# Kernel optimization log

Hardware: AMD Instinct MI355X
Metric: run time of the kernel (lower is better)

Reference implementation:

```python
import jax, jax.numpy as jnp
import numpy as np

LIDAR_MAX_X = 32.0
LIDAR_MAX_Y = 32.0


def bilinear_grid_sample(value, grid):
    """torch.nn.functional.grid_sample, mode='bilinear', padding_mode='zeros',
    align_corners=False.
    value: (B, C, H, W); grid: (B, Q, P, 2) in [-1, 1] (x=width, y=height).
    Returns (B, C, Q, P)."""
    B, C, H, W = value.shape
    x = (grid[..., 0] + 1.0) * (W / 2) - 0.5  # (B,Q,P) unnormalized col
    y = (grid[..., 1] + 1.0) * (H / 2) - 0.5  # (B,Q,P) unnormalized row
    x0 = jnp.floor(x)
    y0 = jnp.floor(y)
    x1 = x0 + 1.0
    y1 = y0 + 1.0
    wx1 = x - x0
    wx0 = 1.0 - wx1
    wy1 = y - y0
    wy0 = 1.0 - wy1
    vflat = value.reshape(B, C, H * W)

    def gather(ix, iy):
        valid = (ix >= 0) & (ix <= W - 1) & (iy >= 0) & (iy <= H - 1)
        ixc = jnp.clip(ix, 0, W - 1).astype(jnp.int32)
        iyc = jnp.clip(iy, 0, H - 1).astype(jnp.int32)
        idx = iyc * W + ixc  # (B,Q,P)
        g = jax.vmap(lambda v, i: v[:, i])(vflat, idx)  # (B,C,Q,P)
        return g * valid[:, None, :, :].astype(value.dtype)

    out = (gather(x0, y0) * (wx0 * wy0)[:, None]
           + gather(x1, y0) * (wx1 * wy0)[:, None]
           + gather(x0, y1) * (wx0 * wy1)[:, None]
           + gather(x1, y1) * (wx1 * wy1)[:, None])
    return out


def setup_inputs() -> dict:
    key = jax.random.key(0)
    ks = jax.random.split(key, 10)
    bs, Q, P, D = 16, 1024, 8, 256
    Cin, H, W = 64, 128, 128
    queries = jax.random.normal(ks[0], (bs, Q, D), dtype=jnp.float32)
    # scale so trajectory points span the +/-32m BEV extent
    traj_points = jax.random.normal(ks[1], (bs, Q, P, 2), dtype=jnp.float32) * 20.0
    bev_feature = jax.random.normal(ks[2], (bs, Cin, H, W), dtype=jnp.float32)
    spatial_shape = jnp.array([H, W], dtype=jnp.int64)
    attn_w = jax.random.normal(ks[3], (P, D), dtype=jnp.float32) * 0.02
    attn_b = jnp.zeros((P,), dtype=jnp.float32)
    conv_w = jax.random.normal(ks[4], (256, Cin, 3, 3), dtype=jnp.float32) * 0.05
    conv_b = jnp.zeros((256,), dtype=jnp.float32)
    out_w = jax.random.normal(ks[5], (D, D), dtype=jnp.float32) * (1.0 / np.sqrt(D))
    out_b = jnp.zeros((D,), dtype=jnp.float32)
    return {"queries": queries, "traj_points": traj_points,
            "bev_feature": bev_feature, "spatial_shape": spatial_shape,
            "attn_w": attn_w, "attn_b": attn_b,
            "conv_w": conv_w, "conv_b": conv_b,
            "out_w": out_w, "out_b": out_b}


def reference(queries, traj_points, bev_feature, spatial_shape,
              attn_w, attn_b, conv_w, conv_b, out_w, out_b):
    # normalize trajectory to [-1,1] and swap (y,x) -> (x,y) grid order
    grid = jnp.stack([traj_points[..., 1] / LIDAR_MAX_X,
                      traj_points[..., 0] / LIDAR_MAX_Y], axis=-1)  # (bs,Q,P,2)
    # per-query attention over the P sampled points
    attn = jax.nn.softmax(
        jnp.einsum('bqd,pd->bqp', queries, attn_w) + attn_b, axis=-1)  # (bs,Q,P)
    # value projection: 3x3 conv + ReLU
    value = jax.lax.conv_general_dilated(
        bev_feature, conv_w, window_strides=(1, 1),
        padding=((1, 1), (1, 1)),
        dimension_numbers=('NCHW', 'OIHW', 'NCHW'))
    value = jax.nn.relu(value + conv_b[None, :, None, None])  # (bs,256,H,W)
    sampled = bilinear_grid_sample(value, grid)  # (bs,256,Q,P)
    out = jnp.einsum('bcqp,bqp->bqc', sampled, attn)  # weighted sum + permute
    out = jnp.einsum('bqc,dc->bqd', out, out_w) + out_b
    # dropout is identity in eval mode
    return out + queries
```

## Files before the change

### kernel.cpp

```cpp
#include <hip/hip_runtime.h>
#include <stdint.h>


typedef __attribute__((ext_vector_type(8))) short short8;
typedef __attribute__((ext_vector_type(4))) float f32x4;

__device__ __forceinline__ unsigned short f2bf(float f) {
  union { float f; unsigned int u; } v; v.f = f;
  unsigned int r = (v.u + 0x7FFFu + ((v.u >> 16) & 1u)) >> 16;
  return (unsigned short)r;
}
__device__ __forceinline__ float bf2f(unsigned short h) {
  union { unsigned int u; float f; } v; v.u = ((unsigned int)h) << 16;
  return v.f;
}

__device__ __forceinline__ void gload_lds16(const void* g, void* l) {
  __builtin_amdgcn_global_load_lds(
      (const __attribute__((address_space(1))) unsigned int*)g,
      (__attribute__((address_space(3))) unsigned int*)l, 16, 0, 0);
}

__global__ __launch_bounds__(256) void k1_transpose(const float* __restrict__ bev,
                                                    unsigned short* __restrict__ nhwc) {
  __shared__ __align__(16) float lds[64 * 32 * 4];
  const int b = blockIdx.x >> 7, y = blockIdx.x & 127;
  const int t = threadIdx.x;
  const float* src = bev + (size_t)(b * 64) * 16384 + y * 128;
#pragma unroll
  for (int k = 0; k < 8; ++k) {
    int chunk = k * 256 + t;
    int ic = chunk >> 5, xq = chunk & 31;
    float4 v = *(const float4*)(src + ic * 16384 + xq * 4);
    int slot = xq ^ (ic >> 3);
    *(float4*)&lds[(ic * 32 + slot) * 4] = v;
  }
  __syncthreads();
  unsigned short* dst = nhwc + (size_t)blockIdx.x * 8192;
#pragma unroll
  for (int k = 0; k < 4; ++k) {
    int co = k * 256 + t;
    int x = co >> 3, icg = co & 7;
    int slot = (x >> 2) ^ icg;
    int w = x & 3;
    uint4 u;
    unsigned int* up = (unsigned int*)&u;
#pragma unroll
    for (int jj = 0; jj < 4; ++jj) {
      float v0 = lds[((icg * 8 + 2 * jj) * 32 + slot) * 4 + w];
      float v1 = lds[((icg * 8 + 2 * jj + 1) * 32 + slot) * 4 + w];
      up[jj] = (unsigned int)f2bf(v0) | ((unsigned int)f2bf(v1) << 16);
    }
    *(uint4*)(dst + x * 64 + icg * 8) = u;
  }
}

__global__ __launch_bounds__(256) void k1b_pack(const float* __restrict__ conv_w,
                                                const float* __restrict__ out_w,
                                                unsigned short* __restrict__ wconv,
                                                unsigned short* __restrict__ wout,
                                                float* __restrict__ zp) {
  const int tid = blockIdx.x * 256 + threadIdx.x;
  for (int idx = tid; idx < 9 * 8 * 256 * 8; idx += 16384) {
    int j = idx & 7, oc = (idx >> 3) & 255, g = (idx >> 11) & 7, o = idx >> 14;
    wconv[idx] = f2bf(conv_w[(oc * 64 + g * 8 + j) * 9 + o]);
  }
  for (int idx = tid; idx < 32 * 256 * 8; idx += 16384) {
    int j = idx & 7, d = (idx >> 3) & 255, g = idx >> 11;
    wout[idx] = f2bf(out_w[d * 256 + g * 8 + j]);
  }
  if (tid < 64) zp[tid] = 0.0f;
}

#define K2_LOADA(s, A) do {                                                   \
    _Pragma("unroll")                                                         \
    for (int ocf_ = 0; ocf_ < 4; ++ocf_)                                      \
      A[ocf_] = gA[(4 * (s) + g) * 256 + wo * 64 + ocf_ * 16 + l15];          \
  } while (0)

#define K2_READB(s, h, B) do {                                                \
    const int o_ = (s) >> 1, ich_ = (s) & 1;                                  \
    const int dyr_ = o_ / 3, dx_ = o_ - dyr_ * 3 - 1;                         \
    _Pragma("unroll")                                                         \
    for (int pf_ = 0; pf_ < 4; ++pf_)                                         \
      B[pf_] = lin[(dyr_ * 8 + ich_ * 4 + g) * 130 + 1 + dx_ +                \
                   ((h) * 4 + pf_) * 16 + l15];                               \
  } while (0)

#define K2_MF(A, B, h) do {                                                   \
    _Pragma("unroll")                                                         \
    for (int ocf_ = 0; ocf_ < 4; ++ocf_)                                      \
      _Pragma("unroll")                                                       \
      for (int pf_ = 0; pf_ < 4; ++pf_)                                       \
        acc[ocf_][(h) * 4 + pf_] = __builtin_amdgcn_mfma_f32_16x16x32_bf16(   \
            A[ocf_], B[pf_], acc[ocf_][(h) * 4 + pf_], 0, 0, 0);              \
  } while (0)

__global__ __launch_bounds__(256, 2) void k2_conv(const unsigned short* __restrict__ nhwc,
                                                  const unsigned short* __restrict__ wconv,
                                                  const float* __restrict__ conv_b,
                                                  const float* __restrict__ zp,
                                                  unsigned short* __restrict__ value) {
  __shared__ __align__(16) char smem[50176];
  const short8* lin = (const short8*)smem;
  const short8* gA = (const short8*)wconv;
  const int bid = blockIdx.x;
  const int swz = (bid & 7) * 256 + (bid >> 3);
  const int b = swz >> 7, y = swz & 127;
  const int t = threadIdx.x, wid = t >> 6, lane = t & 63;
  const int wo = wid;
  const int g = lane >> 4, l15 = lane & 15;

  const unsigned short* bevb = nhwc + (size_t)b * (128 * 128 * 64);
  for (int i = wid; i < 49; i += 4) {
    const int chunk = i * 64 + lane;
    const void* src = (const void*)zp;
    if (chunk < 3120) {
      const int ridx = chunk / 1040;
      const int rem = chunk - ridx * 1040;
      const int icg = rem / 130;
      const int c = rem - icg * 130;
      const int yy = y - 1 + ridx, xx = c - 1;
      if (yy >= 0 && yy < 128 && xx >= 0 && xx < 128)
        src = (const void*)(bevb + ((yy * 128 + xx) * 64 + icg * 8));
    }
    gload_lds16(src, smem + i * 1024);
  }
  __syncthreads();

  const f32x4 z4 = {0.f, 0.f, 0.f, 0.f};
  f32x4 acc[4][8];
#pragma unroll
  for (int i = 0; i < 4; ++i)
#pragma unroll
    for (int j = 0; j < 8; ++j) acc[i][j] = z4;

  short8 A0[4], A1[4], B0[4], B1[4];
  K2_LOADA(0, A0);
  K2_LOADA(1, A1);
  K2_READB(0, 0, B0);
  K2_READB(0, 1, B1);

#pragma unroll
  for (int s = 0; s < 18; ++s) {
    __builtin_amdgcn_s_setprio(1);
    if (s & 1) {
      K2_MF(A1, B0, 0);
      if (s < 17) K2_READB(s + 1, 0, B0);
      K2_MF(A1, B1, 1);
      __builtin_amdgcn_s_setprio(0);
      if (s < 17) K2_READB(s + 1, 1, B1);
      if (s + 2 < 18) K2_LOADA(s + 2, A1);
    } else {
      K2_MF(A0, B0, 0);
      if (s < 17) K2_READB(s + 1, 0, B0);
      K2_MF(A0, B1, 1);
      __builtin_amdgcn_s_setprio(0);
      if (s < 17) K2_READB(s + 1, 1, B1);
      if (s + 2 < 18) K2_LOADA(s + 2, A0);
    }
  }

  unsigned short* vrow = value + (((size_t)(b * 128 + y) * 128 + l15) * 256);
  float4 cb4[4];
#pragma unroll
  for (int ocf = 0; ocf < 4; ++ocf)
    cb4[ocf] = *(const float4*)(conv_b + wo * 64 + ocf * 16 + g * 4);
#pragma unroll
  for (int pf = 0; pf < 8; ++pf) {
#pragma unroll
    for (int ocf = 0; ocf < 4; ++ocf) {
      const int ocb = wo * 64 + ocf * 16 + g * 4;
      ushort4 ov;
      float v0 = acc[ocf][pf][0] + cb4[ocf].x; ov.x = f2bf(v0 > 0.f ? v0 : 0.f);
      float v1 = acc[ocf][pf][1] + cb4[ocf].y; ov.y = f2bf(v1 > 0.f ? v1 : 0.f);
      float v2 = acc[ocf][pf][2] + cb4[ocf].z; ov.z = f2bf(v2 > 0.f ? v2 : 0.f);
      float v3 = acc[ocf][pf][3] + cb4[ocf].w; ov.w = f2bf(v3 > 0.f ? v3 : 0.f);
      *(ushort4*)(vrow + (size_t)pf * 16 * 256 + ocb) = ov;
    }
  }
}

__global__ __launch_bounds__(256) void k3_sample(const float* __restrict__ queries,
                                                 const float* __restrict__ traj,
                                                 const float* __restrict__ attn_w,
                                                 const float* __restrict__ attn_b,
                                                 const unsigned short* __restrict__ value,
                                                 unsigned short* __restrict__ S) {
  const int wid = threadIdx.x >> 6, lane = threadIdx.x & 63;
  const int half = lane >> 5, hl = lane & 31;
  const int bid = blockIdx.x;
  const int sbid = (bid & 7) * 256 + (bid >> 3);
  const int qg = sbid * 8 + wid * 2 + half;
  const int b = qg >> 10;

  const float4 q0 = *(const float4*)(queries + (size_t)qg * 256 + hl * 8);
  const float4 q1 = *(const float4*)(queries + (size_t)qg * 256 + hl * 8 + 4);
  float a[8];
#pragma unroll
  for (int p = 0; p < 8; ++p) {
    const float4 w0 = *(const float4*)(attn_w + p * 256 + hl * 8);
    const float4 w1 = *(const float4*)(attn_w + p * 256 + hl * 8 + 4);
    float d = q0.x * w0.x + q0.y * w0.y + q0.z * w0.z + q0.w * w0.w
            + q1.x * w1.x + q1.y * w1.y + q1.z * w1.z + q1.w * w1.w;
#pragma unroll
    for (int off = 16; off >= 1; off >>= 1) d += __shfl_xor(d, off);
    a[p] = d + attn_b[p];
  }
  float mx = a[0];
#pragma unroll
  for (int p = 1; p < 8; ++p) mx = fmaxf(mx, a[p]);
  float ssum = 0.f;
#pragma unroll
  for (int p = 0; p < 8; ++p) { a[p] = __expf(a[p] - mx); ssum += a[p]; }
  const float inv = 1.f / ssum;

  float acc[8] = {0.f, 0.f, 0.f, 0.f, 0.f, 0.f, 0.f, 0.f};
  const unsigned short* vb = value + (size_t)b * (128 * 128 * 256);
#pragma unroll
  for (int p = 0; p < 8; ++p) {
    const float ty = traj[(qg * 8 + p) * 2 + 0];
    const float tx = traj[(qg * 8 + p) * 2 + 1];
    const float fx = (tx * 0.03125f + 1.f) * 64.f - 0.5f;
    const float fy = (ty * 0.03125f + 1.f) * 64.f - 0.5f;
    const float fx0 = floorf(fx), fy0 = floorf(fy);
    const int ix0 = (int)fx0, iy0 = (int)fy0;
    const float wx1 = fx - fx0, wx0 = 1.f - wx1;
    const float wy1 = fy - fy0, wy0 = 1.f - wy1;
    const float ap = a[p] * inv;
    const float cw[4] = {wx0 * wy0 * ap, wx1 * wy0 * ap, wx0 * wy1 * ap, wx1 * wy1 * ap};
#pragma unroll
    for (int cc = 0; cc < 4; ++cc) {
      const int cx = ix0 + (cc & 1), cy = iy0 + (cc >> 1);
      const bool valid = (cx >= 0) & (cx < 128) & (cy >= 0) & (cy < 128);
      const float w = valid ? cw[cc] : 0.f;
      const int cxc = min(max(cx, 0), 127), cyc = min(max(cy, 0), 127);
      const short8 v = *(const short8*)(vb + (cyc * 128 + cxc) * 256 + hl * 8);
#pragma unroll
      for (int j = 0; j < 8; ++j) acc[j] += w * bf2f((unsigned short)v[j]);
    }
  }
  short8 o;
#pragma unroll
  for (int j = 0; j < 8; ++j) o[j] = (short)f2bf(acc[j]);
  *(short8*)(S + (size_t)qg * 256 + hl * 8) = o;
}

__global__ __launch_bounds__(256) void k4_proj(const unsigned short* __restrict__ S,
                                               const unsigned short* __restrict__ wout,
                                               const float* __restrict__ out_b,
                                               const float* __restrict__ queries,
                                               float* __restrict__ out) {
  const short8* wp8 = (const short8*)wout;
  const short8* Sp = (const short8*)S;
  const int t = threadIdx.x, wid = t >> 6, lane = t & 63;
  const int q0 = blockIdx.x * 64;
  const int g = lane >> 4, l15 = lane & 15;
  const f32x4 z4 = {0.f, 0.f, 0.f, 0.f};
  f32x4 acc[4][4];
#pragma unroll
  for (int i = 0; i < 4; ++i)
#pragma unroll
    for (int j = 0; j < 4; ++j) acc[i][j] = z4;

#pragma unroll
  for (int ks = 0; ks < 8; ++ks) {
    short8 af[4];
#pragma unroll
    for (int df = 0; df < 4; ++df)
      af[df] = wp8[(ks * 4 + g) * 256 + wid * 64 + df * 16 + l15];
    short8 bf[4];
#pragma unroll
    for (int qf = 0; qf < 4; ++qf)
      bf[qf] = Sp[(size_t)(q0 + qf * 16 + l15) * 32 + ks * 4 + g];
#pragma unroll
    for (int df = 0; df < 4; ++df)
#pragma unroll
      for (int qf = 0; qf < 4; ++qf)
        acc[df][qf] = __builtin_amdgcn_mfma_f32_16x16x32_bf16(af[df], bf[qf], acc[df][qf], 0, 0, 0);
  }

#pragma unroll
  for (int df = 0; df < 4; ++df) {
    const int db = wid * 64 + df * 16 + g * 4;
    const float4 ob4 = *(const float4*)(out_b + db);
#pragma unroll
    for (int qf = 0; qf < 4; ++qf) {
      const int q = q0 + qf * 16 + l15;
      const float4 qv = *(const float4*)(queries + (size_t)q * 256 + db);
      float4 ov;
      ov.x = acc[df][qf][0] + ob4.x + qv.x;
      ov.y = acc[df][qf][1] + ob4.y + qv.y;
      ov.z = acc[df][qf][2] + ob4.z + qv.z;
      ov.w = acc[df][qf][3] + ob4.w + qv.w;
      *(float4*)(out + (size_t)q * 256 + db) = ov;
    }
  }
}

extern "C" void kernel_launch(void* const* d_in, const int* in_sizes, int n_in,
                              void* d_out, int out_size, void* d_ws, size_t ws_size,
                              hipStream_t stream) {
  const float* queries = (const float*)d_in[0];
  const float* traj    = (const float*)d_in[1];
  const float* bev     = (const float*)d_in[2];
  const float* attn_w  = (const float*)d_in[4];
  const float* attn_b  = (const float*)d_in[5];
  const float* conv_w  = (const float*)d_in[6];
  const float* conv_b  = (const float*)d_in[7];
  const float* out_w   = (const float*)d_in[8];
  const float* out_b   = (const float*)d_in[9];
  float* out = (float*)d_out;

  char* ws = (char*)d_ws;
  unsigned short* bev_nhwc = (unsigned short*)(ws);
  unsigned short* value    = (unsigned short*)(ws + 33554432);
  unsigned short* wconv    = (unsigned short*)(ws + 167772160);
  unsigned short* wout     = (unsigned short*)(ws + 168067072);
  unsigned short* Sbuf     = (unsigned short*)(ws + 168198144);
  float*          zp       = (float*)(ws + 176586752);

  k1_transpose<<<2048, 256, 0, stream>>>(bev, bev_nhwc);
  k1b_pack<<<64, 256, 0, stream>>>(conv_w, out_w, wconv, wout, zp);
  k2_conv<<<2048, 256, 0, stream>>>(bev_nhwc, wconv, conv_b, zp, value);
  k3_sample<<<2048, 256, 0, stream>>>(queries, traj, attn_w, attn_b, value, Sbuf);
  k4_proj<<<256, 256, 0, stream>>>(Sbuf, wout, out_b, queries, out);
}
```

Baseline: 145.3 us.

## Split conv blocks across output-channel halves to cut registers and raise occupancy

The conv kernel now launches twice as many blocks, each handling half of the 256 output channels for one row. Each wave covers 64 channels by 64 pixels instead of 64 by 128, which halves the accumulator registers and lets launch bounds ask for three blocks per CU. The cost is that every block loads the same three-row input halo into LDS, so input staging traffic doubles. B-operand reads are also no longer prefetched a step ahead and now sit directly before the MFMAs, which may expose LDS latency.

```diff
diff --git a/kernel.cpp b/kernel.cpp
--- a/kernel.cpp
+++ b/kernel.cpp
@@ -75,28 +75,28 @@
 #define K2_LOADA(s, A) do {                                                   \
     _Pragma("unroll")                                                         \
     for (int ocf_ = 0; ocf_ < 4; ++ocf_)                                      \
-      A[ocf_] = gA[(4 * (s) + g) * 256 + wo * 64 + ocf_ * 16 + l15];          \
+      A[ocf_] = gA[(4 * (s) + g) * 256 + ocb0 + ocf_ * 16 + l15];             \
   } while (0)
 
-#define K2_READB(s, h, B) do {                                                \
+#define K2_READB(s, B) do {                                                   \
     const int o_ = (s) >> 1, ich_ = (s) & 1;                                  \
     const int dyr_ = o_ / 3, dx_ = o_ - dyr_ * 3 - 1;                         \
     _Pragma("unroll")                                                         \
     for (int pf_ = 0; pf_ < 4; ++pf_)                                         \
-      B[pf_] = lin[(dyr_ * 8 + ich_ * 4 + g) * 130 + 1 + dx_ +                \
-                   ((h) * 4 + pf_) * 16 + l15];                               \
+      B[pf_] = lin[(dyr_ * 8 + ich_ * 4 + g) * 130 + 1 + dx_ + xb +           \
+                   pf_ * 16 + l15];                                           \
   } while (0)
 
-#define K2_MF(A, B, h) do {                                                   \
+#define K2_MF(A, B) do {                                                      \
     _Pragma("unroll")                                                         \
     for (int ocf_ = 0; ocf_ < 4; ++ocf_)                                      \
       _Pragma("unroll")                                                       \
       for (int pf_ = 0; pf_ < 4; ++pf_)                                       \
-        acc[ocf_][(h) * 4 + pf_] = __builtin_amdgcn_mfma_f32_16x16x32_bf16(   \
-            A[ocf_], B[pf_], acc[ocf_][(h) * 4 + pf_], 0, 0, 0);              \
+        acc[ocf_][pf_] = __builtin_amdgcn_mfma_f32_16x16x32_bf16(             \
+            A[ocf_], B[pf_], acc[ocf_][pf_], 0, 0, 0);                        \
   } while (0)
 
-__global__ __launch_bounds__(256, 2) void k2_conv(const unsigned short* __restrict__ nhwc,
+__global__ __launch_bounds__(256, 3) void k2_conv(const unsigned short* __restrict__ nhwc,
                                                   const unsigned short* __restrict__ wconv,
                                                   const float* __restrict__ conv_b,
                                                   const float* __restrict__ zp,
@@ -105,11 +105,13 @@
   const short8* lin = (const short8*)smem;
   const short8* gA = (const short8*)wconv;
   const int bid = blockIdx.x;
-  const int swz = (bid & 7) * 256 + (bid >> 3);
-  const int b = swz >> 7, y = swz & 127;
+  const int swz = (bid & 7) * 512 + (bid >> 3);
+  const int b = swz >> 8, y = (swz >> 1) & 127, och = swz & 1;
   const int t = threadIdx.x, wid = t >> 6, lane = t & 63;
-  const int wo = wid;
+  const int wo = wid >> 1;
+  const int xb = (wid & 1) * 64;
   const int g = lane >> 4, l15 = lane & 15;
+  const int ocb0 = och * 128 + wo * 64;
 
   const unsigned short* bevb = nhwc + (size_t)b * (128 * 128 * 64);
   for (int i = wid; i < 49; i += 4) {
@@ -129,48 +131,41 @@
   __syncthreads();
 
   const f32x4 z4 = {0.f, 0.f, 0.f, 0.f};
-  f32x4 acc[4][8];
+  f32x4 acc[4][4];
 #pragma unroll
   for (int i = 0; i < 4; ++i)
 #pragma unroll
-    for (int j = 0; j < 8; ++j) acc[i][j] = z4;
-
-  short8 A0[4], A1[4], B0[4], B1[4];
+    for (int j = 0; j < 4; ++j) acc[i][j] = z4;
+
+  short8 A0[4], A1[4], B[4];
   K2_LOADA(0, A0);
   K2_LOADA(1, A1);
-  K2_READB(0, 0, B0);
-  K2_READB(0, 1, B1);
 
 #pragma unroll
   for (int s = 0; s < 18; ++s) {
+    K2_READB(s, B);
     __builtin_amdgcn_s_setprio(1);
     if (s & 1) {
-      K2_MF(A1, B0, 0);
-      if (s < 17) K2_READB(s + 1, 0, B0);
-      K2_MF(A1, B1, 1);
+      K2_MF(A1, B);
       __builtin_amdgcn_s_setprio(0);
-      if (s < 17) K2_READB(s + 1, 1, B1);
       if (s + 2 < 18) K2_LOADA(s + 2, A1);
     } else {
-      K2_MF(A0, B0, 0);
-      if (s < 17) K2_READB(s + 1, 0, B0);
-      K2_MF(A0, B1, 1);
+      K2_MF(A0, B);
       __builtin_amdgcn_s_setprio(0);
-      if (s < 17) K2_READB(s + 1, 1, B1);
       if (s + 2 < 18) K2_LOADA(s + 2, A0);
     }
   }
 
-  unsigned short* vrow = value + (((size_t)(b * 128 + y) * 128 + l15) * 256);
+  unsigned short* vrow = value + (((size_t)(b * 128 + y) * 128 + xb + l15) * 256);
   float4 cb4[4];
 #pragma unroll
   for (int ocf = 0; ocf < 4; ++ocf)
-    cb4[ocf] = *(const float4*)(conv_b + wo * 64 + ocf * 16 + g * 4);
-#pragma unroll
-  for (int pf = 0; pf < 8; ++pf) {
+    cb4[ocf] = *(const float4*)(conv_b + ocb0 + ocf * 16 + g * 4);
+#pragma unroll
+  for (int pf = 0; pf < 4; ++pf) {
 #pragma unroll
     for (int ocf = 0; ocf < 4; ++ocf) {
-      const int ocb = wo * 64 + ocf * 16 + g * 4;
+      const int ocb = ocb0 + ocf * 16 + g * 4;
       ushort4 ov;
       float v0 = acc[ocf][pf][0] + cb4[ocf].x; ov.x = f2bf(v0 > 0.f ? v0 : 0.f);
       float v1 = acc[ocf][pf][1] + cb4[ocf].y; ov.y = f2bf(v1 > 0.f ? v1 : 0.f);
@@ -322,7 +317,7 @@
 
   k1_transpose<<<2048, 256, 0, stream>>>(bev, bev_nhwc);
   k1b_pack<<<64, 256, 0, stream>>>(conv_w, out_w, wconv, wout, zp);
-  k2_conv<<<2048, 256, 0, stream>>>(bev_nhwc, wconv, conv_b, zp, value);
+  k2_conv<<<4096, 256, 0, stream>>>(bev_nhwc, wconv, conv_b, zp, value);
   k3_sample<<<2048, 256, 0, stream>>>(queries, traj, attn_w, attn_b, value, Sbuf);
   k4_proj<<<256, 256, 0, stream>>>(Sbuf, wout, out_b, queries, out);
 }
```

Result: slower. 161.4 us (+11.1%).
